# Kernel optimization log

Hardware: AMD Instinct MI355X
Metric: run time of the kernel (lower is better)

The kernel has to match this reference:

```python
import jax, jax.numpy as jnp
import numpy as np

HEADS = 4
DHEAD = 64
S = 16  # reduce_size (and rel-pos `shape`)

_DN = ('NCHW', 'OIHW', 'NCHW')

def dsconv(x, dw, pw):
    # depthwise 3x3 (groups=C, pad 1, no bias) then pointwise 1x1 (no bias)
    g = dw.shape[0]
    y = jax.lax.conv_general_dilated(x, dw, (1, 1), ((1, 1), (1, 1)),
                                     dimension_numbers=_DN, feature_group_count=g)
    return jax.lax.conv_general_dilated(y, pw, (1, 1), ((0, 0), (0, 0)),
                                        dimension_numbers=_DN)

def setup_inputs() -> dict:
    key = jax.random.key(0)
    ks = jax.random.split(key, 7)
    B, C, H, W = 4, 256, 128, 128
    inner = HEADS * DHEAD  # 256
    x = jax.random.normal(ks[0], (B, C, H, W), jnp.float32)
    dw1 = jax.random.normal(ks[1], (C, 1, 3, 3), jnp.float32) * 0.05
    pw1 = jax.random.normal(ks[2], (3 * inner, C, 1, 1), jnp.float32) * 0.05
    key_rel_w = jax.random.normal(ks[3], (2 * S - 1, DHEAD), jnp.float32) * 0.02
    key_rel_h = jax.random.normal(ks[4], (2 * S - 1, DHEAD), jnp.float32) * 0.02
    dw2 = jax.random.normal(ks[5], (inner, 1, 3, 3), jnp.float32) * 0.05
    pw2 = jax.random.normal(ks[6], (C, inner, 1, 1), jnp.float32) * 0.05
    return dict(x=x, dw1=dw1, pw1=pw1, key_rel_w=key_rel_w, key_rel_h=key_rel_h,
                dw2=dw2, pw2=pw2)

def reference(x, dw1, pw1, key_rel_w, key_rel_h, dw2, pw2):
    B, C, H, W = x.shape
    inner = HEADS * DHEAD
    scale = DHEAD ** (-0.5)

    qkv = dsconv(x, dw1, pw1)                      # (B, 3*inner, H, W)
    q, k, v = jnp.split(qkv, 3, axis=1)

    # adaptive max pool to (S,S): H,W divisible by S -> plain max pool
    kh, kw = H // S, W // S
    pool = lambda t: jax.lax.reduce_window(t, -jnp.inf, jax.lax.max,
                                           (1, 1, kh, kw), (1, 1, kh, kw), 'VALID')
    k, v = pool(k), pool(v)

    # torch rearrange 'b (dim_head heads) h w -> b heads (h w) dim_head'
    # i.e. channel c = dh*heads + head
    def to_heads(t, h, w):
        return t.reshape(B, DHEAD, HEADS, h * w).transpose(0, 2, 3, 1)
    q = to_heads(q, H, W)                          # (B, Nh, H*W, d)
    k = to_heads(k, S, S)                          # (B, Nh, S*S, d)
    v = to_heads(v, S, S)

    qk = jnp.einsum('bhid,bhjd->bhij', q, k)       # (B, Nh, H*W, S*S)

    # --- relative position bias (gather-based, 1d factored) ---
    coords = jnp.arange(S)
    rel_idx = coords[None, :] - coords[:, None] + (S - 1)    # (S, S)
    q5 = q.reshape(B, HEADS, H, W, DHEAD)
    # width logits
    logits_w = jnp.einsum('bhxyd,md->bhxym', q5, key_rel_w)  # (B,Nh,H,W,2S-1)
    idx_w = jnp.broadcast_to(jnp.repeat(rel_idx, W // S, axis=0)[None, None, None],
                             (B, HEADS, H, W, S))
    gw = jnp.take_along_axis(logits_w, idx_w, axis=4)        # (B,Nh,H,W,S) keyed by w
    # height logits (q transposed so rows are W, cols are H)
    qp = q5.transpose(0, 1, 3, 2, 4)                         # (B,Nh,W,H,d)
    logits_h = jnp.einsum('bhxyd,md->bhxym', qp, key_rel_h)  # (B,Nh,W,H,2S-1)
    idx_h = jnp.broadcast_to(jnp.repeat(rel_idx, H // S, axis=0)[None, None, None],
                             (B, HEADS, W, H, S))
    gh = jnp.take_along_axis(logits_h, idx_h, axis=4)        # (B,Nh,W,H,S)
    gh = gh.transpose(0, 1, 3, 2, 4)                         # (B,Nh,H,W,S) keyed by h
    # bias[b,nh,(Hq,Wq),(hk,wk)] = gh[...,hk] + gw[...,wk]
    bias = (gh[..., :, None] + gw[..., None, :]).reshape(B, HEADS, H * W, S * S)

    attn = jax.nn.softmax((qk + bias) * scale, axis=-1)
    out = jnp.einsum('bhij,bhjd->bhid', attn, v)             # (B,Nh,H*W,d)
    # 'b heads (h w) dim_head -> b (dim_head heads) h w'
    out = out.transpose(0, 3, 1, 2).reshape(B, inner, H, W)
    out = dsconv(out, dw2, pw2)
    return out, attn
```

## Files before the change

kernel.cpp:

```cpp
#include <hip/hip_runtime.h>

#define HW 16384
#define CH 256

__global__ __launch_bounds__(256) void k_dw(const float* __restrict__ in,
                                            const float* __restrict__ w,
                                            float* __restrict__ out) {
  int bc = blockIdx.x;
  int c = bc & 255;
  float wv[9];
#pragma unroll
  for (int i = 0; i < 9; ++i) wv[i] = w[c * 9 + i];
  const float* ip = in + (size_t)bc * HW;
  float* op = out + (size_t)bc * HW;
  int t = threadIdx.x;
  for (int r = 0; r < 64; ++r) {
    int pix = r * 256 + t;
    int y = pix >> 7, x = pix & 127;
    float s = 0.f;
#pragma unroll
    for (int dy = 0; dy < 3; ++dy) {
      int yy = y + dy - 1;
      if (yy < 0 || yy > 127) continue;
#pragma unroll
      for (int dx = 0; dx < 3; ++dx) {
        int xx = x + dx - 1;
        if (xx < 0 || xx > 127) continue;
        s += wv[dy * 3 + dx] * ip[yy * 128 + xx];
      }
    }
    op[pix] = s;
  }
}

__global__ __launch_bounds__(256) void k_pw(const float* __restrict__ T,
                                            const float* __restrict__ Wt,
                                            float* __restrict__ o0,
                                            float* __restrict__ o1,
                                            float* __restrict__ o2) {
  __shared__ __align__(16) float As[16][128];
  __shared__ __align__(16) float Bs[16][128];
  int b = blockIdx.z;
  int n0 = blockIdx.x * 128;
  int gm0 = blockIdx.y * 128;
  int sel = blockIdx.y >> 1;
  float* outp = sel == 0 ? o0 : (sel == 1 ? o1 : o2);
  int lm0 = (blockIdx.y & 1) * 128;
  const float* Tb = T + (size_t)b * CH * HW;
  int t = threadIdx.x;
  int ty = t >> 4, tx = t & 15;
  int arow = t >> 1, af4 = (t & 1) * 2;
  int bk = t >> 5, bf4 = t & 31;
  float acc[8][8] = {};
  for (int k0 = 0; k0 < 256; k0 += 16) {
    __syncthreads();
#pragma unroll
    for (int ii = 0; ii < 2; ++ii) {
      float4 a4 = *(const float4*)(Wt + (size_t)(gm0 + arow) * 256 + k0 + (af4 + ii) * 4);
      As[(af4 + ii) * 4 + 0][arow] = a4.x;
      As[(af4 + ii) * 4 + 1][arow] = a4.y;
      As[(af4 + ii) * 4 + 2][arow] = a4.z;
      As[(af4 + ii) * 4 + 3][arow] = a4.w;
    }
#pragma unroll
    for (int ii = 0; ii < 2; ++ii) {
      *(float4*)&Bs[ii * 8 + bk][bf4 * 4] =
          *(const float4*)(Tb + (size_t)(k0 + ii * 8 + bk) * HW + n0 + bf4 * 4);
    }
    __syncthreads();
#pragma unroll
    for (int kk = 0; kk < 16; ++kk) {
      float4 a0 = *(const float4*)&As[kk][ty * 4];
      float4 a1 = *(const float4*)&As[kk][64 + ty * 4];
      float4 b0 = *(const float4*)&Bs[kk][tx * 4];
      float4 b1 = *(const float4*)&Bs[kk][64 + tx * 4];
      float av[8] = {a0.x, a0.y, a0.z, a0.w, a1.x, a1.y, a1.z, a1.w};
      float bv[8] = {b0.x, b0.y, b0.z, b0.w, b1.x, b1.y, b1.z, b1.w};
#pragma unroll
      for (int i = 0; i < 8; ++i)
#pragma unroll
        for (int j = 0; j < 8; ++j) acc[i][j] += av[i] * bv[j];
    }
  }
#pragma unroll
  for (int ih = 0; ih < 2; ++ih)
#pragma unroll
    for (int i = 0; i < 4; ++i) {
      int lrow = lm0 + ih * 64 + ty * 4 + i;
#pragma unroll
      for (int jh = 0; jh < 2; ++jh) {
        float4 o;
        o.x = acc[ih * 4 + i][jh * 4 + 0]; o.y = acc[ih * 4 + i][jh * 4 + 1];
        o.z = acc[ih * 4 + i][jh * 4 + 2]; o.w = acc[ih * 4 + i][jh * 4 + 3];
        *(float4*)(outp + ((size_t)b * CH + lrow) * HW + n0 + jh * 64 + tx * 4) = o;
      }
    }
}

__global__ __launch_bounds__(256) void k_pool(const float* __restrict__ src,
                                              float* __restrict__ dst) {
  int idx = blockIdx.x * 256 + threadIdx.x;
  int cell = idx & 255;
  int c = (idx >> 8) & 255;
  int b = idx >> 16;
  int sy = cell >> 4, sx = cell & 15;
  const float* sp = src + ((size_t)b * CH + c) * HW + (sy * 8) * 128 + sx * 8;
  float m = -1e30f;
#pragma unroll
  for (int iy = 0; iy < 8; ++iy) {
    float4 v0 = *(const float4*)(sp + iy * 128);
    float4 v1 = *(const float4*)(sp + iy * 128 + 4);
    m = fmaxf(m, fmaxf(fmaxf(v0.x, v0.y), fmaxf(v0.z, v0.w)));
    m = fmaxf(m, fmaxf(fmaxf(v1.x, v1.y), fmaxf(v1.z, v1.w)));
  }
  int dh = c >> 2, head = c & 3;
  dst[((size_t)(b * 4 + head) * 256 + cell) * 64 + dh] = m;
}

__global__ __launch_bounds__(256) void k_poolT(const float* __restrict__ src,
                                               float* __restrict__ dst) {
  int idx = blockIdx.x * 256 + threadIdx.x;
  int cell = idx & 255;
  int c = (idx >> 8) & 255;
  int b = idx >> 16;
  int sy = cell >> 4, sx = cell & 15;
  const float* sp = src + ((size_t)b * CH + c) * HW + (sy * 8) * 128 + sx * 8;
  float m = -1e30f;
#pragma unroll
  for (int iy = 0; iy < 8; ++iy) {
    float4 v0 = *(const float4*)(sp + iy * 128);
    float4 v1 = *(const float4*)(sp + iy * 128 + 4);
    m = fmaxf(m, fmaxf(fmaxf(v0.x, v0.y), fmaxf(v0.z, v0.w)));
    m = fmaxf(m, fmaxf(fmaxf(v1.x, v1.y), fmaxf(v1.z, v1.w)));
  }
  int dh = c >> 2, head = c & 3;
  dst[((size_t)(b * 4 + head) * 64 + dh) * 256 + cell] = m;
}

__global__ __launch_bounds__(256, 3) void k_attn(
    const float* __restrict__ q, const float* __restrict__ kp,
    const float* __restrict__ vp, const float* __restrict__ relh,
    const float* __restrict__ relw, float* __restrict__ attn_o,
    float* __restrict__ ao) {
  int tile = blockIdx.x, head = blockIdx.y, b = blockIdx.z;
  int t = threadIdx.x;
  int pix0 = tile * 64;
  int bh = b * 4 + head;
  const size_t kvb = (size_t)bh * 16384;

  __shared__ __align__(16) float sm[10304];
  float* u1 = sm;
  float* u2 = sm + 4160;
  float* rhw = sm + 8256;

  int ty = t >> 4, tx = t & 15;

  {
    int dq = t >> 4, f4 = t & 15;
#pragma unroll
    for (int i = 0; i < 4; ++i) {
      int d = i * 16 + dq;
      *(float4*)&u1[d * 64 + f4 * 4] =
          *(const float4*)(q + ((size_t)(b * CH + d * 4 + head)) * HW + pix0 + f4 * 4);
    }
  }
  for (int e = t; e < 3968; e += 256) {
    int tab = e >= 1984 ? 1 : 0;
    int e2 = tab ? e - 1984 : e;
    int row = e2 >> 6, d = e2 & 63;
    u2[tab * 2015 + row * 65 + d] = tab ? relw[e2] : relh[e2];
  }
  __syncthreads();

  {
    int pp = t >> 2, mg = t & 3;
    int pixel = pix0 + pp;
    int y = pixel >> 7, x = pixel & 127;
    int ybase = 15 - (y >> 3), xbase = 15 - (x >> 3);
    int roff[8];
#pragma unroll
    for (int mm = 0; mm < 8; ++mm) {
      int m = mg * 8 + mm;
      roff[mm] = (m < 16) ? (m + ybase) * 65 : 2015 + (m - 16 + xbase) * 65;
    }
    float s[8] = {};
#pragma unroll 4
    for (int d = 0; d < 64; ++d) {
      float qv = u1[d * 64 + pp];
#pragma unroll
      for (int mm = 0; mm < 8; ++mm) s[mm] += qv * u2[roff[mm] + d];
    }
#pragma unroll
    for (int mm = 0; mm < 8; ++mm) rhw[pp * 32 + mg * 8 + mm] = s[mm];
  }

  float L[4][16] = {};
#pragma unroll
  for (int qk = 0; qk < 4; ++qk) {
    __syncthreads();
    {
      int dq = t >> 4, f4 = t & 15;
#pragma unroll
      for (int i = 0; i < 4; ++i) {
        int d = i * 16 + dq;
        *(float4*)&u2[d * 64 + f4 * 4] =
            *(const float4*)(kp + kvb + (size_t)d * 256 + qk * 64 + f4 * 4);
      }
    }
    __syncthreads();
#pragma unroll 8
    for (int d = 0; d < 64; ++d) {
      float4 qv = *(const float4*)&u1[d * 64 + ty * 4];
      float4 kv4 = *(const float4*)&u2[d * 64 + tx * 4];
      float qa[4] = {qv.x, qv.y, qv.z, qv.w};
      float ka[4] = {kv4.x, kv4.y, kv4.z, kv4.w};
#pragma unroll
      for (int i = 0; i < 4; ++i)
#pragma unroll
        for (int j = 0; j < 4; ++j) L[i][qk * 4 + j] += qa[i] * ka[j];
    }
  }

#pragma unroll
  for (int i = 0; i < 4; ++i) {
    int pp = ty * 4 + i;
    float m_ = -1e30f;
#pragma unroll
    for (int qk = 0; qk < 4; ++qk) {
      int hk = qk * 4 + (tx >> 2);
      float gh = rhw[pp * 32 + hk];
#pragma unroll
      for (int j = 0; j < 4; ++j) {
        int wk = (tx * 4 + j) & 15;
        float v = (L[i][qk * 4 + j] + gh + rhw[pp * 32 + 16 + wk]) * 0.125f;
        L[i][qk * 4 + j] = v;
        m_ = fmaxf(m_, v);
      }
    }
    m_ = fmaxf(m_, __shfl_xor(m_, 1));
    m_ = fmaxf(m_, __shfl_xor(m_, 2));
    m_ = fmaxf(m_, __shfl_xor(m_, 4));
    m_ = fmaxf(m_, __shfl_xor(m_, 8));
    float s_ = 0.f;
#pragma unroll
    for (int k2 = 0; k2 < 16; ++k2) {
      float e = __expf(L[i][k2] - m_);
      L[i][k2] = e;
      s_ += e;
    }
    s_ += __shfl_xor(s_, 1);
    s_ += __shfl_xor(s_, 2);
    s_ += __shfl_xor(s_, 4);
    s_ += __shfl_xor(s_, 8);
    float inv = 1.f / s_;
#pragma unroll
    for (int k2 = 0; k2 < 16; ++k2) L[i][k2] *= inv;
  }

#pragma unroll
  for (int i = 0; i < 4; ++i) {
    float* arow = attn_o + ((size_t)bh * HW + pix0 + ty * 4 + i) * 256 + tx * 4;
#pragma unroll
    for (int qk = 0; qk < 4; ++qk) {
      float4 o;
      o.x = L[i][qk * 4 + 0]; o.y = L[i][qk * 4 + 1];
      o.z = L[i][qk * 4 + 2]; o.w = L[i][qk * 4 + 3];
      *(float4*)(arow + qk * 64) = o;
    }
  }

  float acc2[4][4] = {};
#pragma unroll
  for (int qk = 0; qk < 4; ++qk) {
    __syncthreads();
#pragma unroll
    for (int i = 0; i < 4; ++i) {
      int idx = i * 256 + t;
      *(float4*)&u2[idx * 4] = *(const float4*)(vp + kvb + (size_t)qk * 4096 + idx * 4);
    }
#pragma unroll
    for (int i = 0; i < 4; ++i)
#pragma unroll
      for (int j = 0; j < 4; ++j)
        u1[(tx * 4 + j) * 65 + i * 16 + ty] = L[i][qk * 4 + j];
    __syncthreads();
#pragma unroll 8
    for (int kk = 0; kk < 64; ++kk) {
      float4 vv = *(const float4*)&u2[kk * 64 + ty * 4];
      float va[4] = {vv.x, vv.y, vv.z, vv.w};
      float pa[4];
#pragma unroll
      for (int i = 0; i < 4; ++i) pa[i] = u1[kk * 65 + i * 16 + tx];
#pragma unroll
      for (int dd = 0; dd < 4; ++dd)
#pragma unroll
        for (int i = 0; i < 4; ++i) acc2[dd][i] += pa[i] * va[dd];
    }
  }

#pragma unroll
  for (int dd = 0; dd < 4; ++dd) {
    int ch = (ty * 4 + dd) * 4 + head;
    float4 o;
    o.x = acc2[dd][0]; o.y = acc2[dd][1]; o.z = acc2[dd][2]; o.w = acc2[dd][3];
    *(float4*)(ao + ((size_t)b * CH + ch) * HW + pix0 + tx * 4) = o;
  }
}

extern "C" void kernel_launch(void* const* d_in, const int* in_sizes, int n_in,
                              void* d_out, int out_size, void* d_ws, size_t ws_size,
                              hipStream_t stream) {
  const float* x   = (const float*)d_in[0];
  const float* dw1 = (const float*)d_in[1];
  const float* pw1 = (const float*)d_in[2];
  const float* krw = (const float*)d_in[3];
  const float* krh = (const float*)d_in[4];
  const float* dw2 = (const float*)d_in[5];
  const float* pw2 = (const float*)d_in[6];

  float* out = (float*)d_out;
  float* attnbuf = out + (size_t)16777216;

  float* t1    = attnbuf;
  float* kfull = attnbuf + (size_t)16777216;
  float* vfull = attnbuf + (size_t)33554432;
  float* qb = (float*)d_ws;
  float* kp = qb + (size_t)16777216;
  float* vp = kp + (size_t)262144;
  float* t2 = qb;

  dim3 b256(256);
  k_dw<<<dim3(1024), b256, 0, stream>>>(x, dw1, t1);
  k_pw<<<dim3(128, 6, 4), b256, 0, stream>>>(t1, pw1, qb, kfull, vfull);
  k_poolT<<<dim3(1024), b256, 0, stream>>>(kfull, kp);
  k_pool<<<dim3(1024), b256, 0, stream>>>(vfull, vp);
  k_attn<<<dim3(256, 4, 4), b256, 0, stream>>>(qb, kp, vp, krh, krw, attnbuf, out);
  k_dw<<<dim3(1024), b256, 0, stream>>>(out, dw2, t2);
  k_pw<<<dim3(128, 2, 4), b256, 0, stream>>>(t2, pw2, out, out, out);
}
```

Before: 1.312 ms.

## Vectorize depthwise conv, prefetch GEMM tiles, and restructure attention shared memory

The depthwise 3x3 kernel now computes four adjacent pixels per thread using float4 row loads plus two edge scalars. The pointwise GEMM doubles the K tile to 32 and prefetches the next tile into registers while computing the current one, with launch bounds set to 2 blocks per SM. The attention kernel stops staging the relative-position tables in shared memory and reads them from global with float4 loads. It also stores the probability tile in a padded row-major layout with vectorized writes, and raises its occupancy hint to 4 blocks. This cuts per-thread load instructions and synchronisation overhead, at the cost of more register pressure and more global or cache traffic for the rel-pos tables.

Measured after the change: 3.386 ms. 2.58x slower.

```diff
diff --git a/kernel.cpp b/kernel.cpp
--- a/kernel.cpp
+++ b/kernel.cpp
@@ -14,32 +14,37 @@
   const float* ip = in + (size_t)bc * HW;
   float* op = out + (size_t)bc * HW;
   int t = threadIdx.x;
-  for (int r = 0; r < 64; ++r) {
-    int pix = r * 256 + t;
-    int y = pix >> 7, x = pix & 127;
-    float s = 0.f;
+  for (int r = 0; r < 16; ++r) {
+    int q4 = r * 256 + t;
+    int pix = q4 * 4;
+    int y = pix >> 7, x0 = pix & 127;
+    float ax = 0.f, ay = 0.f, az = 0.f, aw = 0.f;
 #pragma unroll
     for (int dy = 0; dy < 3; ++dy) {
       int yy = y + dy - 1;
       if (yy < 0 || yy > 127) continue;
-#pragma unroll
-      for (int dx = 0; dx < 3; ++dx) {
-        int xx = x + dx - 1;
-        if (xx < 0 || xx > 127) continue;
-        s += wv[dy * 3 + dx] * ip[yy * 128 + xx];
-      }
-    }
-    op[pix] = s;
-  }
-}
-
-__global__ __launch_bounds__(256) void k_pw(const float* __restrict__ T,
-                                            const float* __restrict__ Wt,
-                                            float* __restrict__ o0,
-                                            float* __restrict__ o1,
-                                            float* __restrict__ o2) {
-  __shared__ __align__(16) float As[16][128];
-  __shared__ __align__(16) float Bs[16][128];
+      const float* row = ip + yy * 128 + x0;
+      float4 cv = *(const float4*)row;
+      float lf = (x0 > 0) ? row[-1] : 0.f;
+      float rt = (x0 < 124) ? row[4] : 0.f;
+      float w0 = wv[dy * 3 + 0], w1 = wv[dy * 3 + 1], w2 = wv[dy * 3 + 2];
+      ax += w0 * lf   + w1 * cv.x + w2 * cv.y;
+      ay += w0 * cv.x + w1 * cv.y + w2 * cv.z;
+      az += w0 * cv.y + w1 * cv.z + w2 * cv.w;
+      aw += w0 * cv.z + w1 * cv.w + w2 * rt;
+    }
+    float4 o; o.x = ax; o.y = ay; o.z = az; o.w = aw;
+    *(float4*)(op + pix) = o;
+  }
+}
+
+__global__ __launch_bounds__(256, 2) void k_pw(const float* __restrict__ T,
+                                               const float* __restrict__ Wt,
+                                               float* __restrict__ o0,
+                                               float* __restrict__ o1,
+                                               float* __restrict__ o2) {
+  __shared__ __align__(16) float As[32][128];
+  __shared__ __align__(16) float Bs[32][128];
   int b = blockIdx.z;
   int n0 = blockIdx.x * 128;
   int gm0 = blockIdx.y * 128;
@@ -49,27 +54,36 @@
   const float* Tb = T + (size_t)b * CH * HW;
   int t = threadIdx.x;
   int ty = t >> 4, tx = t & 15;
-  int arow = t >> 1, af4 = (t & 1) * 2;
-  int bk = t >> 5, bf4 = t & 31;
+  int arow = t >> 1, acol = (t & 1) * 16;
+  int brow = t >> 3, bcol = (t & 7) * 16;
+  const float* aptr = Wt + (size_t)(gm0 + arow) * 256 + acol;
+  const float* bptr = Tb + (size_t)brow * HW + n0 + bcol;
+  float4 ra[4], rb[4];
+#pragma unroll
+  for (int i = 0; i < 4; ++i) {
+    ra[i] = *(const float4*)(aptr + i * 4);
+    rb[i] = *(const float4*)(bptr + i * 4);
+  }
   float acc[8][8] = {};
-  for (int k0 = 0; k0 < 256; k0 += 16) {
-    __syncthreads();
-#pragma unroll
-    for (int ii = 0; ii < 2; ++ii) {
-      float4 a4 = *(const float4*)(Wt + (size_t)(gm0 + arow) * 256 + k0 + (af4 + ii) * 4);
-      As[(af4 + ii) * 4 + 0][arow] = a4.x;
-      As[(af4 + ii) * 4 + 1][arow] = a4.y;
-      As[(af4 + ii) * 4 + 2][arow] = a4.z;
-      As[(af4 + ii) * 4 + 3][arow] = a4.w;
-    }
-#pragma unroll
-    for (int ii = 0; ii < 2; ++ii) {
-      *(float4*)&Bs[ii * 8 + bk][bf4 * 4] =
-          *(const float4*)(Tb + (size_t)(k0 + ii * 8 + bk) * HW + n0 + bf4 * 4);
-    }
-    __syncthreads();
-#pragma unroll
-    for (int kk = 0; kk < 16; ++kk) {
+  for (int k0 = 0; k0 < 256; k0 += 32) {
+#pragma unroll
+    for (int i = 0; i < 4; ++i) {
+      As[acol + i * 4 + 0][arow] = ra[i].x;
+      As[acol + i * 4 + 1][arow] = ra[i].y;
+      As[acol + i * 4 + 2][arow] = ra[i].z;
+      As[acol + i * 4 + 3][arow] = ra[i].w;
+      *(float4*)&Bs[brow][bcol + i * 4] = rb[i];
+    }
+    __syncthreads();
+    if (k0 + 32 < 256) {
+#pragma unroll
+      for (int i = 0; i < 4; ++i) {
+        ra[i] = *(const float4*)(aptr + k0 + 32 + i * 4);
+        rb[i] = *(const float4*)(bptr + (size_t)(k0 + 32) * HW + i * 4);
+      }
+    }
+#pragma unroll
+    for (int kk = 0; kk < 32; ++kk) {
       float4 a0 = *(const float4*)&As[kk][ty * 4];
       float4 a1 = *(const float4*)&As[kk][64 + ty * 4];
       float4 b0 = *(const float4*)&Bs[kk][tx * 4];
@@ -81,6 +95,7 @@
 #pragma unroll
         for (int j = 0; j < 8; ++j) acc[i][j] += av[i] * bv[j];
     }
+    __syncthreads();
   }
 #pragma unroll
   for (int ih = 0; ih < 2; ++ih)
@@ -137,7 +152,7 @@
   dst[((size_t)(b * 4 + head) * 64 + dh) * 256 + cell] = m;
 }
 
-__global__ __launch_bounds__(256, 3) void k_attn(
+__global__ __launch_bounds__(256, 4) void k_attn(
     const float* __restrict__ q, const float* __restrict__ kp,
     const float* __restrict__ vp, const float* __restrict__ relh,
     const float* __restrict__ relw, float* __restrict__ attn_o,
@@ -148,10 +163,10 @@
   int bh = b * 4 + head;
   const size_t kvb = (size_t)bh * 16384;
 
-  __shared__ __align__(16) float sm[10304];
+  __shared__ __align__(16) float sm[10240];
   float* u1 = sm;
-  float* u2 = sm + 4160;
-  float* rhw = sm + 8256;
+  float* rhw = sm + 4096;
+  float* u2 = sm + 6144;
 
   int ty = t >> 4, tx = t & 15;
 
@@ -163,12 +178,6 @@
       *(float4*)&u1[d * 64 + f4 * 4] =
           *(const float4*)(q + ((size_t)(b * CH + d * 4 + head)) * HW + pix0 + f4 * 4);
     }
-  }
-  for (int e = t; e < 3968; e += 256) {
-    int tab = e >= 1984 ? 1 : 0;
-    int e2 = tab ? e - 1984 : e;
-    int row = e2 >> 6, d = e2 & 63;
-    u2[tab * 2015 + row * 65 + d] = tab ? relw[e2] : relh[e2];
   }
   __syncthreads();
 
@@ -177,18 +186,27 @@
     int pixel = pix0 + pp;
     int y = pixel >> 7, x = pixel & 127;
     int ybase = 15 - (y >> 3), xbase = 15 - (x >> 3);
-    int roff[8];
+    const float* rb[8];
 #pragma unroll
     for (int mm = 0; mm < 8; ++mm) {
       int m = mg * 8 + mm;
-      roff[mm] = (m < 16) ? (m + ybase) * 65 : 2015 + (m - 16 + xbase) * 65;
+      rb[mm] = (m < 16) ? (relh + (m + ybase) * 64) : (relw + (m - 16 + xbase) * 64);
     }
     float s[8] = {};
-#pragma unroll 4
-    for (int d = 0; d < 64; ++d) {
-      float qv = u1[d * 64 + pp];
-#pragma unroll
-      for (int mm = 0; mm < 8; ++mm) s[mm] += qv * u2[roff[mm] + d];
+#pragma unroll
+    for (int dc = 0; dc < 4; ++dc) {
+      float qreg[16];
+#pragma unroll
+      for (int dd = 0; dd < 16; ++dd) qreg[dd] = u1[(dc * 16 + dd) * 64 + pp];
+#pragma unroll
+      for (int mm = 0; mm < 8; ++mm) {
+#pragma unroll
+        for (int d4 = 0; d4 < 4; ++d4) {
+          float4 rv = *(const float4*)(rb[mm] + dc * 16 + d4 * 4);
+          s[mm] += qreg[d4 * 4 + 0] * rv.x + qreg[d4 * 4 + 1] * rv.y +
+                   qreg[d4 * 4 + 2] * rv.z + qreg[d4 * 4 + 3] * rv.w;
+        }
+      }
     }
 #pragma unroll
     for (int mm = 0; mm < 8; ++mm) rhw[pp * 32 + mg * 8 + mm] = s[mm];
@@ -279,22 +297,30 @@
       *(float4*)&u2[idx * 4] = *(const float4*)(vp + kvb + (size_t)qk * 4096 + idx * 4);
     }
 #pragma unroll
-    for (int i = 0; i < 4; ++i)
-#pragma unroll
-      for (int j = 0; j < 4; ++j)
-        u1[(tx * 4 + j) * 65 + i * 16 + ty] = L[i][qk * 4 + j];
-    __syncthreads();
-#pragma unroll 8
-    for (int kk = 0; kk < 64; ++kk) {
-      float4 vv = *(const float4*)&u2[kk * 64 + ty * 4];
-      float va[4] = {vv.x, vv.y, vv.z, vv.w};
-      float pa[4];
-#pragma unroll
-      for (int i = 0; i < 4; ++i) pa[i] = u1[kk * 65 + i * 16 + tx];
-#pragma unroll
-      for (int dd = 0; dd < 4; ++dd)
-#pragma unroll
-        for (int i = 0; i < 4; ++i) acc2[dd][i] += pa[i] * va[dd];
+    for (int i = 0; i < 4; ++i) {
+      float4 pv;
+      pv.x = L[i][qk * 4 + 0]; pv.y = L[i][qk * 4 + 1];
+      pv.z = L[i][qk * 4 + 2]; pv.w = L[i][qk * 4 + 3];
+      *(float4*)&u1[(ty * 4 + i) * 68 + tx * 4] = pv;
+    }
+    __syncthreads();
+#pragma unroll
+    for (int kq = 0; kq < 16; ++kq) {
+#pragma unroll
+      for (int jp = 0; jp < 2; ++jp) {
+        float4 v0 = *(const float4*)&u2[(kq * 4 + jp * 2 + 0) * 64 + ty * 4];
+        float4 v1 = *(const float4*)&u2[(kq * 4 + jp * 2 + 1) * 64 + ty * 4];
+        float va0[4] = {v0.x, v0.y, v0.z, v0.w};
+        float va1[4] = {v1.x, v1.y, v1.z, v1.w};
+#pragma unroll
+        for (int i = 0; i < 4; ++i) {
+          float p0 = u1[(tx * 4 + i) * 68 + kq * 4 + jp * 2 + 0];
+          float p1 = u1[(tx * 4 + i) * 68 + kq * 4 + jp * 2 + 1];
+#pragma unroll
+          for (int dd = 0; dd < 4; ++dd)
+            acc2[dd][i] += p0 * va0[dd] + p1 * va1[dd];
+        }
+      }
     }
   }
 
```
